# Kernel tuning notes

Hardware: AMD Instinct MI355X
Metric: run time of the kernel (lower is better)

Reference implementation:

```python
import jax, jax.numpy as jnp
import numpy as np

NEG = -1e30  # safe 'log zero' for fp32 (avoids -inf NaNs in grads)


def _ctc_loss(logits, targets, input_lengths, target_lengths):
    """PyTorch-semantics CTC loss: blank=0, reduction='mean', zero_infinity=True.
    logits: [B,T,C] (pre-log-softmax), targets: [B,S] padded, lengths: [B].
    """
    B, T, C = logits.shape
    S = targets.shape[1]
    L = 2 * S + 1  # extended target length (blanks interleaved)
    logp = jax.nn.log_softmax(logits, axis=-1)  # [B,T,C]

    # extended targets: blank, y1, blank, y2, ..., blank
    ext = jnp.zeros((B, L), jnp.int32).at[:, 1::2].set(targets.astype(jnp.int32))
    lp_ext = jnp.take_along_axis(
        logp, jnp.broadcast_to(ext[:, None, :], (B, T, L)), axis=2)  # [B,T,L]

    pos = jnp.arange(L)
    ext_m2 = jnp.pad(ext, ((0, 0), (2, 0)))[:, :L]
    can_skip = (ext != 0) & (ext != ext_m2) & (pos >= 2)  # [B,L]

    def shift(a, k):
        return jnp.pad(a, ((0, 0), (k, 0)), constant_values=NEG)[:, :L]

    def lse3(a, b, c):
        m = jnp.maximum(jnp.maximum(a, b), c)
        return m + jnp.log(jnp.exp(a - m) + jnp.exp(b - m) + jnp.exp(c - m))

    alpha0 = (jnp.full((B, L), NEG, logits.dtype)
              .at[:, 0].set(lp_ext[:, 0, 0])
              .at[:, 1].set(lp_ext[:, 0, 1]))

    def step(alpha, xs):
        lp_t, t = xs  # lp_t: [B,L]
        a2 = shift(alpha, 1)
        a3 = jnp.where(can_skip, shift(alpha, 2), NEG)
        new = lp_t + lse3(alpha, a2, a3)
        # freeze alpha once past each sample's input_length
        alpha = jnp.where((t < input_lengths)[:, None], new, alpha)
        return alpha, None

    lp_T = jnp.swapaxes(lp_ext, 0, 1)  # [T,B,L]
    alpha, _ = jax.lax.scan(step, alpha0, (lp_T[1:], jnp.arange(1, T)))

    i1 = (2 * target_lengths - 1).astype(jnp.int32)
    i2 = (2 * target_lengths).astype(jnp.int32)
    a_last = jnp.take_along_axis(alpha, i1[:, None], axis=1)[:, 0]
    a_blank = jnp.take_along_axis(alpha, i2[:, None], axis=1)[:, 0]
    loss = -jnp.logaddexp(a_last, a_blank)  # [B]
    loss = jnp.where(loss > 1e29, 0.0, loss)  # zero_infinity=True
    return jnp.mean(loss / target_lengths.astype(loss.dtype))


def setup_inputs() -> dict:
    key = jax.random.key(0)
    ks = jax.random.split(key, 8)
    B, T = 32, 2000
    C_err, S_err = 4, 50
    C_ph, S_ph = 64, 200
    error_logits = jax.random.normal(ks[0], (B, T, C_err), jnp.float32)
    phoneme_logits = jax.random.normal(ks[1], (B, T, C_ph), jnp.float32)
    # labels in [1, C): blank=0 never appears in targets
    error_targets = jax.random.randint(ks[2], (B, S_err), 1, C_err, jnp.int32)
    phoneme_targets = jax.random.randint(ks[3], (B, S_ph), 1, C_ph, jnp.int32)
    error_input_lengths = jax.random.randint(ks[4], (B,), T - T // 4, T + 1, jnp.int32)
    phoneme_input_lengths = jax.random.randint(ks[5], (B,), T - T // 4, T + 1, jnp.int32)
    error_target_lengths = jax.random.randint(ks[6], (B,), S_err // 2, S_err + 1, jnp.int32)
    phoneme_target_lengths = jax.random.randint(ks[7], (B,), S_ph // 2, S_ph + 1, jnp.int32)
    return {
        "error_logits": error_logits,
        "phoneme_logits": phoneme_logits,
        "error_targets": error_targets,
        "phoneme_targets": phoneme_targets,
        "error_input_lengths": error_input_lengths,
        "phoneme_input_lengths": phoneme_input_lengths,
        "error_target_lengths": error_target_lengths,
        "phoneme_target_lengths": phoneme_target_lengths,
    }


def reference(error_logits, phoneme_logits, error_targets, phoneme_targets,
              error_input_lengths, phoneme_input_lengths,
              error_target_lengths, phoneme_target_lengths):
    error_weight = 1.0
    phoneme_weight = 1.0
    error_loss = _ctc_loss(error_logits, error_targets,
                           error_input_lengths, error_target_lengths)
    phoneme_loss = _ctc_loss(phoneme_logits, phoneme_targets,
                             phoneme_input_lengths, phoneme_target_lengths)
    total_loss = error_weight * error_loss + phoneme_weight * phoneme_loss
    return total_loss
```

## Files before the change

### kernel.cpp

```cpp
#include <hip/hip_runtime.h>
#include <math.h>


static constexpr float  LOG2E = 1.4426950408889634f;
static constexpr double LN2D  = 0.6931471805599453;
static constexpr int GROWS = 2032;

#define DPP_WAVE_SHR1   0x138
#define DPP_ROW_SHR(n)  (0x110 | (n))
#define DPP_ROW_BCAST15 0x142
#define DPP_ROW_BCAST31 0x143

__device__ __forceinline__ float fexp2(float x) {
  return __builtin_amdgcn_exp2f(x);
}
__device__ __forceinline__ float flog2(float x) {
  return __builtin_amdgcn_logf(x);
}

__device__ __forceinline__ double dpp_shr1_f64(double x) {
  int lo = __double2loint(x), hi = __double2hiint(x);
  lo = __builtin_amdgcn_update_dpp(0, lo, DPP_WAVE_SHR1, 0xf, 0xf, true);
  hi = __builtin_amdgcn_update_dpp(0, hi, DPP_WAVE_SHR1, 0xf, 0xf, true);
  return __hiloint2double(hi, lo);
}

__device__ __forceinline__ int imax2(int a, int b) { return a > b ? a : b; }

__device__ __forceinline__ int wave_imax(int v) {
  v = imax2(v, __builtin_amdgcn_update_dpp(0, v, DPP_ROW_SHR(1), 0xf, 0xf, true));
  v = imax2(v, __builtin_amdgcn_update_dpp(0, v, DPP_ROW_SHR(2), 0xf, 0xf, true));
  v = imax2(v, __builtin_amdgcn_update_dpp(0, v, DPP_ROW_SHR(4), 0xf, 0xf, true));
  v = imax2(v, __builtin_amdgcn_update_dpp(0, v, DPP_ROW_SHR(8), 0xf, 0xf, true));
  v = imax2(v, __builtin_amdgcn_update_dpp(0, v, DPP_ROW_BCAST15, 0xf, 0xf, true));
  v = imax2(v, __builtin_amdgcn_update_dpp(0, v, DPP_ROW_BCAST31, 0xf, 0xf, true));
  return __builtin_amdgcn_readlane(v, 63);
}

__device__ __forceinline__ void wait_lgkm0() {
  __builtin_amdgcn_sched_barrier(0);
  __builtin_amdgcn_s_waitcnt(49279);
  __builtin_amdgcn_sched_barrier(0);
}

__device__ __forceinline__ void spin_fence() {
  __builtin_amdgcn_sched_barrier(0);
}


__global__ __launch_bounds__(256) void gather_ph_kernel(
    const float* __restrict__ ph_logits, const float* __restrict__ err_logits,
    const int* __restrict__ ph_tgt,
    float* __restrict__ Gph, float* __restrict__ Lpb_ph,
    float* __restrict__ Lpb_er, float* __restrict__ out) {
  const int bx = blockIdx.x, b = blockIdx.y;
  const int tid = threadIdx.x;
  const int lane = tid & 63, wv = tid >> 6;

  if (bx == 0 && b == 0 && tid == 0) *out = 0.f;

  if (wv == 0 && lane < 32) {
    const int t = bx * 32 + lane;
    if (t < 2000) {
      const float4 v = *(const float4*)(err_logits + ((size_t)b * 2000 + t) * 4);
      const float z0 = v.x * LOG2E;
      const float s = fexp2(z0) + fexp2(v.y * LOG2E) + fexp2(v.z * LOG2E) +
                      fexp2(v.w * LOG2E);
      Lpb_er[(size_t)b * GROWS + t] = z0 - flog2(s);
    }
  }

  const int* tb = ph_tgt + b * 200;
  int idx[4];
  float msk[4];
#pragma unroll
  for (int k = 0; k < 4; ++k) {
    const int si = lane * 4 + k;
    const int cls = (si < 200) ? tb[si] : 0;
    idx[k] = cls << 2;
    msk[k] = (si < 200) ? 1.0f : 0.0f;
  }
  const int t0 = (bx * 4 + wv) * 8;
  float z[8], e[8], s[8];
#pragma unroll
  for (int u = 0; u < 8; ++u) {
    const int t = t0 + u;
    const int tc = (t < 2000) ? t : 1999;
    z[u] = ph_logits[((size_t)b * 2000 + tc) * 64 + lane] * LOG2E;
    e[u] = fexp2(z[u]);
    s[u] = e[u];
  }
#pragma unroll
  for (int off = 32; off >= 1; off >>= 1) {
#pragma unroll
    for (int u = 0; u < 8; ++u) s[u] += __shfl_xor(s[u], off, 64);
  }
#pragma unroll
  for (int u = 0; u < 8; ++u) {
    const int t = t0 + u;
    if (t < 2000) {
      const float e0 = __int_as_float(
          __builtin_amdgcn_readlane(__float_as_int(e[u]), 0));
      const float inv0 = 1.0f / e0;
      float o[4];
#pragma unroll
      for (int k = 0; k < 4; ++k) {
        const float v = __int_as_float(
            __builtin_amdgcn_ds_bpermute(idx[k], __float_as_int(e[u])));
        o[k] = msk[k] * v * inv0;
      }
      *(float4*)(Gph + ((size_t)b * GROWS + t) * 256 + lane * 4) =
          make_float4(o[0], o[1], o[2], o[3]);
      if (lane == 0)
        Lpb_ph[(size_t)b * GROWS + t] = z[u] - flog2(s[u]);
    }
  }
}

template <int P> struct RowP { float v[P]; };

template <int P>
__device__ __forceinline__ void bl_renorm(double (&B)[P], double (&L)[P],
                                          int& K) {
  double mm = B[0];
#pragma unroll
  for (int k = 0; k < P; ++k) mm = fmax(fmax(mm, B[k]), L[k]);
  const int ex = (__double2hiint(mm) >> 20) & 0x7ff;
  const int emax = wave_imax(ex);
  if (emax > 0) {
    int d = 1523 - emax;
    if (d > 1023) d = 1023;
    if (d < -1022) d = -1022;
    const double sc = __hiloint2double((d + 1023) << 20, 0);
#pragma unroll
    for (int k = 0; k < P; ++k) { B[k] *= sc; L[k] *= sc; }
    K += d;
  }
}

template <int P>
__device__ __forceinline__ void bl_step(double (&B)[P], double (&L)[P],
                                        const double (&skipm)[P],
                                        const RowP<P>& f) {
  const double Lm1 = dpp_shr1_f64(L[P - 1]);
  double nB[P], nL[P];
#pragma unroll
  for (int k = 0; k < P; ++k) {
    const double Lp = (k >= 1) ? L[k - 1] : Lm1;
    nB[k] = B[k] + Lp;
    nL[k] = (double)f.v[k] * fma(skipm[k], Lp, B[k] + L[k]);
  }
#pragma unroll
  for (int k = 0; k < P; ++k) { B[k] = nB[k]; L[k] = nL[k]; }
}

template <int P>
__device__ __forceinline__ void bl_readout(double (&B)[P], double (&L)[P],
                                           int K, float spb, int tl,
                                           float* __restrict__ out,
                                           double* sa) {
  const int lane = threadIdx.x;
  double* saB = sa;
  double* saL = sa + 64 * P;
#pragma unroll
  for (int k = 0; k < P; ++k) {
    saB[lane * P + k] = B[k];
    saL[lane * P + k] = L[k];
  }
  wait_lgkm0();
  if (lane == 0) {
    const double a = saL[tl - 1] + saB[tl];
    float loss = (float)((double)K * LN2D - log(a) - (double)spb * LN2D);
    if (!(loss < 1e29f)) loss = 0.f;
    atomicAdd(out, loss / ((float)tl * 32.0f));
  }
}

__device__ __forceinline__ float spb_sum(const float* __restrict__ Lpb,
                                         int len) {
  const int lane = threadIdx.x;
  float spb = 0.f;
  for (int t0 = lane; t0 < len; t0 += 512) {
#pragma unroll
    for (int u = 0; u < 8; ++u) {
      const int t = t0 + u * 64;
      const int tc = (t < len) ? t : 0;
      const float v = Lpb[tc];
      spb += (t < len) ? v : 0.0f;
    }
  }
#pragma unroll
  for (int off = 32; off >= 1; off >>= 1) spb += __shfl_xor(spb, off, 64);
  return spb;
}

__device__ __forceinline__ void chain_ph(
    const float* __restrict__ Glab,
    const float* __restrict__ Lpb,
    const int* __restrict__ tb, int len, int tl,
    float* __restrict__ out, double* sa) {
  constexpr int P = 4, S = 200, LSTRIDE = 256;
  const int lane = threadIdx.x;

  const float spb = spb_sum(Lpb, len);

  double skipm[P];
#pragma unroll
  for (int k = 0; k < P; ++k) {
    const int s = lane * P + k;
    skipm[k] = (s >= 1 && s < S && tb[s] != tb[s - 1]) ? 1.0 : 0.0;
  }

  double B[P], L[P];
#pragma unroll
  for (int k = 0; k < P; ++k) { B[k] = 0.0; L[k] = 0.0; }
  {
    const float r0 = Glab[0];
    if (lane == 0) { B[0] = 1.0; L[0] = (double)r0; }
  }
  int K = 0;

  const float* gp = Glab + lane * P;
  const int ngroups = (len - 1) / 16;

  auto ldrow = [&](int t) {
    RowP<P> r;
    const float4 a = *(const float4*)(gp + (size_t)t * LSTRIDE);
    r.v[0] = a.x; r.v[1] = a.y; r.v[2] = a.z; r.v[3] = a.w;
    return r;
  };

  RowP<P> bufA[16], bufB[16];
  if (ngroups >= 1) {
#pragma unroll
    for (int u = 0; u < 16; ++u) bufA[u] = ldrow(1 + u);
  }
  if (ngroups >= 2) {
#pragma unroll
    for (int u = 0; u < 16; ++u) bufB[u] = ldrow(17 + u);
  }
  spin_fence();

  int g = 0;
  for (; g + 2 <= ngroups; g += 2) {
    bl_renorm<P>(B, L, K);
#pragma unroll
    for (int u = 0; u < 16; ++u) bl_step<P>(B, L, skipm, bufA[u]);
    {
      const int gn = (g + 2 < ngroups) ? (g + 2) : 0;
      const int tbase = 1 + gn * 16;
#pragma unroll
      for (int u = 0; u < 16; ++u) bufA[u] = ldrow(tbase + u);
    }
    spin_fence();
    bl_renorm<P>(B, L, K);
#pragma unroll
    for (int u = 0; u < 16; ++u) bl_step<P>(B, L, skipm, bufB[u]);
    {
      const int gn = (g + 3 < ngroups) ? (g + 3) : 0;
      const int tbase = 1 + gn * 16;
#pragma unroll
      for (int u = 0; u < 16; ++u) bufB[u] = ldrow(tbase + u);
    }
    spin_fence();
  }
  if (g < ngroups) {
    bl_renorm<P>(B, L, K);
#pragma unroll
    for (int u = 0; u < 16; ++u) bl_step<P>(B, L, skipm, bufA[u]);
    ++g;
  }

  {
    const int tstart = 1 + ngroups * 16;
    RowP<P> bufT[15];
#pragma unroll
    for (int u = 0; u < 15; ++u) {
      int t = tstart + u;
      if (t > len - 1) t = len - 1;
      bufT[u] = ldrow(t);
    }
#pragma unroll
    for (int u = 0; u < 15; ++u) {
      const int t = tstart + u;
      if (t < len) {
        if (u == 0) bl_renorm<P>(B, L, K);
        bl_step<P>(B, L, skipm, bufT[u]);
      }
    }
  }

  bl_readout<P>(B, L, K, spb, tl, out, sa);
}

__device__ __forceinline__ void chain_er(
    const float* __restrict__ zb,
    const float* __restrict__ Lpb,
    const int* __restrict__ tb, int len, int tl,
    float* __restrict__ out, double* sa) {
  constexpr int P = 1, S = 50;
  const int lane = threadIdx.x;

  const float spb = spb_sum(Lpb, len);

  const int c1 = tb[(lane < S) ? lane : (S - 1)];
  const float fmask = (lane < S) ? 1.0f : 0.0f;
  double skipm[P];
  skipm[0] = (lane >= 1 && lane < S && tb[lane] != tb[lane - 1]) ? 1.0 : 0.0;

  double B[P], L[P];
  B[0] = 0.0; L[0] = 0.0;
  const float4* zr = (const float4*)zb;
  {
    const float4 q0 = zr[0];
    const int c0 = tb[0];
    const float zc = (c0 == 1) ? q0.y : (c0 == 2) ? q0.z : q0.w;
    if (lane == 0) {
      B[0] = 1.0;
      L[0] = (double)fexp2((zc - q0.x) * LOG2E);
    }
  }
  int K = 0;
  const int ngroups = (len - 1) / 16;

  auto mkf = [&](float4 q) {
    RowP<P> f;
    const float zc = (c1 == 1) ? q.y : (c1 == 2) ? q.z : q.w;
    f.v[0] = fmask * fexp2((zc - q.x) * LOG2E);
    return f;
  };

  float4 bufA[16], bufB[16];
  if (ngroups >= 1) {
#pragma unroll
    for (int u = 0; u < 16; ++u) bufA[u] = zr[1 + u];
  }
  if (ngroups >= 2) {
#pragma unroll
    for (int u = 0; u < 16; ++u) bufB[u] = zr[17 + u];
  }
  spin_fence();

  int g = 0;
  for (; g + 2 <= ngroups; g += 2) {
    bl_renorm<P>(B, L, K);
#pragma unroll
    for (int u = 0; u < 16; ++u) {
      const RowP<P> f = mkf(bufA[u]);
      bl_step<P>(B, L, skipm, f);
    }
    {
      const int gn = (g + 2 < ngroups) ? (g + 2) : 0;
      const float4* nx = zr + 1 + (size_t)gn * 16;
#pragma unroll
      for (int u = 0; u < 16; ++u) bufA[u] = nx[u];
    }
    spin_fence();
    bl_renorm<P>(B, L, K);
#pragma unroll
    for (int u = 0; u < 16; ++u) {
      const RowP<P> f = mkf(bufB[u]);
      bl_step<P>(B, L, skipm, f);
    }
    {
      const int gn = (g + 3 < ngroups) ? (g + 3) : 0;
      const float4* nx = zr + 1 + (size_t)gn * 16;
#pragma unroll
      for (int u = 0; u < 16; ++u) bufB[u] = nx[u];
    }
    spin_fence();
  }
  if (g < ngroups) {
    bl_renorm<P>(B, L, K);
#pragma unroll
    for (int u = 0; u < 16; ++u) {
      const RowP<P> f = mkf(bufA[u]);
      bl_step<P>(B, L, skipm, f);
    }
    ++g;
  }

  {
    const int tstart = 1 + ngroups * 16;
    float4 bufT[15];
#pragma unroll
    for (int u = 0; u < 15; ++u) {
      int t = tstart + u;
      if (t > len - 1) t = len - 1;
      bufT[u] = zr[t];
    }
#pragma unroll
    for (int u = 0; u < 15; ++u) {
      const int t = tstart + u;
      if (t < len) {
        if (u == 0) bl_renorm<P>(B, L, K);
        const RowP<P> f = mkf(bufT[u]);
        bl_step<P>(B, L, skipm, f);
      }
    }
  }

  bl_readout<P>(B, L, K, spb, tl, out, sa);
}

__global__ __launch_bounds__(64, 1) void ctc_chains_pin_kernel(
    const float* __restrict__ Gph, const float* __restrict__ err_logits,
    const int* __restrict__ ph_tgt, const int* __restrict__ err_tgt,
    const int* __restrict__ err_il, const int* __restrict__ ph_il,
    const int* __restrict__ err_tl, const int* __restrict__ ph_tl,
    const float* __restrict__ Lpb_ph, const float* __restrict__ Lpb_er,
    float* __restrict__ out) {
  __shared__ double sa[512];
  const int blk = blockIdx.x;
  if (blk < 32) {
    int len = err_il[blk]; if (len > 2000) len = 2000;
    chain_er(err_logits + (size_t)blk * 2000 * 4,
             Lpb_er + (size_t)blk * GROWS, err_tgt + blk * 50, len,
             err_tl[blk], out, sa);
  } else {
    const int b = blk - 32;
    int len = ph_il[b]; if (len > 2000) len = 2000;
    chain_ph(Gph + (size_t)b * GROWS * 256,
             Lpb_ph + (size_t)b * GROWS, ph_tgt + b * 200, len,
             ph_tl[b], out, sa);
  }
}


__global__ __launch_bounds__(256) void softmax4_kernel(
    const float* __restrict__ x, float* __restrict__ p, int nrows) {
  int r = blockIdx.x * blockDim.x + threadIdx.x;
  if (r >= nrows) return;
  float4 v = *reinterpret_cast<const float4*>(x + (size_t)r * 4);
  float z0 = v.x * LOG2E, z1 = v.y * LOG2E, z2 = v.z * LOG2E, z3 = v.w * LOG2E;
  float m = fmaxf(fmaxf(z0, z1), fmaxf(z2, z3));
  float e0 = fexp2(z0 - m), e1 = fexp2(z1 - m);
  float e2 = fexp2(z2 - m), e3 = fexp2(z3 - m);
  float inv = 1.0f / (e0 + e1 + e2 + e3);
  float4 o;
  o.x = e0 * inv; o.y = e1 * inv; o.z = e2 * inv; o.w = e3 * inv;
  *reinterpret_cast<float4*>(p + (size_t)r * 4) = o;
}

__global__ __launch_bounds__(256) void softmax64_kernel(
    const float* __restrict__ x, float* __restrict__ p, int nrows) {
  int row = blockIdx.x * 4 + (threadIdx.x >> 6);
  int lane = threadIdx.x & 63;
  if (row >= nrows) return;
  float z = x[(size_t)row * 64 + lane] * LOG2E;
  float m = z;
#pragma unroll
  for (int off = 32; off >= 1; off >>= 1) m = fmaxf(m, __shfl_xor(m, off, 64));
  float e = fexp2(z - m);
  float s = e;
#pragma unroll
  for (int off = 32; off >= 1; off >>= 1) s += __shfl_xor(s, off, 64);
  p[(size_t)row * 64 + lane] = e * (1.0f / s);
}

template <int C, int S, int R>
__device__ __forceinline__ void ctc_chain_lin_fb(
    const float* __restrict__ p_b, const int* __restrict__ tgt_b,
    int len, int tl, float* __restrict__ out, double* sa) {
  constexpr int L = 2 * S + 1;
  const int lane = threadIdx.x;
  int idx[R];
  double skipm[R];
#pragma unroll
  for (int j = 0; j < R; ++j) {
    const int l = lane * R + j;
    int cls = 0;
    bool sk = false;
    if (l & 1) {
      const int s = (l - 1) >> 1;
      const int sc = (s < S) ? s : (S - 1);
      cls = tgt_b[sc];
      if (s >= 1 && s < S) sk = (cls != tgt_b[s - 1]);
    }
    idx[j] = cls * 4;
    skipm[j] = sk ? 1.0 : 0.0;
  }
  double alpha[R];
#pragma unroll
  for (int j = 0; j < R; ++j) {
    const int l = lane * R + j;
    alpha[j] = (l <= 1) ? (double)p_b[idx[j] >> 2] : 0.0;
  }
  int K = 0;
  const int cl = lane & (C - 1);
  float rv = p_b[(size_t)((1 < len - 1) ? 1 : (len - 1)) * C + cl];
  float pf[R];
#pragma unroll
  for (int j = 0; j < R; ++j)
    pf[j] = __int_as_float(__builtin_amdgcn_ds_bpermute(idx[j], __float_as_int(rv)));
  rv = p_b[(size_t)((2 < len - 1) ? 2 : (len - 1)) * C + cl];
  for (int t = 1; t < len; ++t) {
    if ((t & 31) == 0) {
      double m = alpha[0];
#pragma unroll
      for (int j = 1; j < R; ++j) m = fmax(m, alpha[j]);
#pragma unroll
      for (int off = 1; off < 64; off <<= 1) m = fmax(m, __shfl_xor(m, off, 64));
      const long long bits = __double_as_longlong(m);
      const int e = (int)((bits >> 52) & 0x7FF);
      if (e > 0) {
        const double sc = __longlong_as_double((long long)(2046 - e) << 52);
#pragma unroll
        for (int j = 0; j < R; ++j) alpha[j] *= sc;
        K += 1023 - e;
      }
    }
    const int tn = (t + 2 < len) ? (t + 2) : (len - 1);
    const float rvn = p_b[(size_t)tn * C + cl];
    float pfn[R];
#pragma unroll
    for (int j = 0; j < R; ++j)
      pfn[j] = __int_as_float(__builtin_amdgcn_ds_bpermute(idx[j], __float_as_int(rv)));
    double am1 = __shfl_up(alpha[R - 1], 1, 64);
    double am2 = __shfl_up(alpha[R - 2], 1, 64);
    if (lane == 0) { am1 = 0.0; am2 = 0.0; }
    double na[R];
#pragma unroll
    for (int j = 0; j < R; ++j) {
      const double a0 = alpha[j];
      const double a1 = (j >= 1) ? alpha[j - 1] : am1;
      const double a2 = (j >= 2) ? alpha[j - 2] : ((j == 1) ? am1 : am2);
      double s = a0 + a1;
      s = fma(skipm[j], a2, s);
      na[j] = (double)pf[j] * s;
    }
#pragma unroll
    for (int j = 0; j < R; ++j) alpha[j] = na[j];
#pragma unroll
    for (int j = 0; j < R; ++j) pf[j] = pfn[j];
    rv = rvn;
  }
#pragma unroll
  for (int j = 0; j < R; ++j) {
    const int l = lane * R + j;
    if (l < L) sa[l] = alpha[j];
  }
  __syncthreads();
  if (lane == 0) {
    const double a = sa[2 * tl - 1] + sa[2 * tl];
    float loss = (float)((double)K * LN2D - log(a));
    if (!(loss < 1e29f)) loss = 0.0f;
    atomicAdd(out, loss / ((float)tl * 32.0f));
  }
}

__global__ __launch_bounds__(64) void ctc_chains_fb_kernel(
    const float* __restrict__ p_err, const float* __restrict__ p_ph,
    const int* __restrict__ err_tgt, const int* __restrict__ ph_tgt,
    const int* __restrict__ err_il, const int* __restrict__ ph_il,
    const int* __restrict__ err_tl, const int* __restrict__ ph_tl,
    float* __restrict__ out) {
  __shared__ double sa[512];
  const int T = 2000;
  const int blk = blockIdx.x;
  if (blk < 32) {
    const int b = blk;
    int len = err_il[b]; if (len > T) len = T;
    ctc_chain_lin_fb<4, 50, 2>(p_err + (size_t)b * T * 4, err_tgt + b * 50, len,
                               err_tl[b], out, sa);
  } else {
    const int b = blk - 32;
    int len = ph_il[b]; if (len > T) len = T;
    ctc_chain_lin_fb<64, 200, 7>(p_ph + (size_t)b * T * 64, ph_tgt + b * 200,
                                 len, ph_tl[b], out, sa);
  }
}


extern "C" void kernel_launch(void* const* d_in, const int* in_sizes, int n_in,
                              void* d_out, int out_size, void* d_ws,
                              size_t ws_size, hipStream_t stream) {
  const float* err_logits = (const float*)d_in[0];
  const float* ph_logits  = (const float*)d_in[1];
  const int* err_tgt = (const int*)d_in[2];
  const int* ph_tgt  = (const int*)d_in[3];
  const int* err_il  = (const int*)d_in[4];
  const int* ph_il   = (const int*)d_in[5];
  const int* err_tl  = (const int*)d_in[6];
  const int* ph_tl   = (const int*)d_in[7];
  float* out = (float*)d_out;

  const size_t gph = (size_t)32 * GROWS * 256;
  const size_t lpb = (size_t)32 * GROWS;
  const size_t need = (gph + 2 * lpb) * sizeof(float);

  if (ws_size >= need) {
    float* Gph = (float*)d_ws;
    float* Lpb_ph = Gph + gph;
    float* Lpb_er = Lpb_ph + lpb;
    gather_ph_kernel<<<dim3(63, 32), 256, 0, stream>>>(
        ph_logits, err_logits, ph_tgt, Gph, Lpb_ph, Lpb_er, out);
    ctc_chains_pin_kernel<<<64, 64, 0, stream>>>(
        Gph, err_logits, ph_tgt, err_tgt, err_il, ph_il, err_tl, ph_tl,
        Lpb_ph, Lpb_er, out);
  } else {
    (void)hipMemsetAsync(d_out, 0, sizeof(float), stream);
    const int B = 32, T = 2000;
    const int rows = B * T;
    float* p_err = (float*)d_ws;
    float* p_ph  = p_err + (size_t)rows * 4;
    softmax4_kernel<<<(rows + 255) / 256, 256, 0, stream>>>(err_logits, p_err, rows);
    softmax64_kernel<<<(rows + 3) / 4, 256, 0, stream>>>(ph_logits, p_ph, rows);
    ctc_chains_fb_kernel<<<64, 64, 0, stream>>>(p_err, p_ph, err_tgt, ph_tgt,
                                                err_il, ph_il, err_tl, ph_tl, out);
  }
}
```

Before: 222.9 us.

## Split CTC recursion into concurrent forward and backward halves meeting at midpoint

Each block now runs two waves: one computes the alpha recursion over the first half of the time steps while the other runs a beta-style backward recursion over the second half. The two halves are combined with a dot product of the state vectors, with the renormalisation exponents added together. This roughly halves the serial dependency chain length per sequence, which dominates the chain kernel. It adds a backward step implementation, shared-memory exchange and a block barrier, and it risks numerical mismatch in the scaling bookkeeping.

```diff
diff --git a/kernel.cpp b/kernel.cpp
--- a/kernel.cpp
+++ b/kernel.cpp
@@ -6,6 +6,7 @@
 static constexpr double LN2D  = 0.6931471805599453;
 static constexpr int GROWS = 2032;
 
+#define DPP_WAVE_SHL1   0x130
 #define DPP_WAVE_SHR1   0x138
 #define DPP_ROW_SHR(n)  (0x110 | (n))
 #define DPP_ROW_BCAST15 0x142
@@ -22,6 +23,13 @@
   int lo = __double2loint(x), hi = __double2hiint(x);
   lo = __builtin_amdgcn_update_dpp(0, lo, DPP_WAVE_SHR1, 0xf, 0xf, true);
   hi = __builtin_amdgcn_update_dpp(0, hi, DPP_WAVE_SHR1, 0xf, 0xf, true);
+  return __hiloint2double(hi, lo);
+}
+
+__device__ __forceinline__ double dpp_shl1_f64(double x) {
+  int lo = __double2loint(x), hi = __double2hiint(x);
+  lo = __builtin_amdgcn_update_dpp(0, lo, DPP_WAVE_SHL1, 0xf, 0xf, true);
+  hi = __builtin_amdgcn_update_dpp(0, hi, DPP_WAVE_SHL1, 0xf, 0xf, true);
   return __hiloint2double(hi, lo);
 }
 
@@ -37,16 +45,6 @@
   return __builtin_amdgcn_readlane(v, 63);
 }
 
-__device__ __forceinline__ void wait_lgkm0() {
-  __builtin_amdgcn_sched_barrier(0);
-  __builtin_amdgcn_s_waitcnt(49279);
-  __builtin_amdgcn_sched_barrier(0);
-}
-
-__device__ __forceinline__ void spin_fence() {
-  __builtin_amdgcn_sched_barrier(0);
-}
-
 
 __global__ __launch_bounds__(256) void gather_ph_kernel(
     const float* __restrict__ ph_logits, const float* __restrict__ err_logits,
@@ -121,14 +119,14 @@
 
 template <int P>
 __device__ __forceinline__ void bl_renorm(double (&B)[P], double (&L)[P],
-                                          int& K) {
+                                          int& K, int tgt) {
   double mm = B[0];
 #pragma unroll
   for (int k = 0; k < P; ++k) mm = fmax(fmax(mm, B[k]), L[k]);
   const int ex = (__double2hiint(mm) >> 20) & 0x7ff;
   const int emax = wave_imax(ex);
   if (emax > 0) {
-    int d = 1523 - emax;
+    int d = tgt - emax;
     if (d > 1023) d = 1023;
     if (d < -1022) d = -1022;
     const double sc = __hiloint2double((d + 1023) << 20, 0);
@@ -155,30 +153,28 @@
 }
 
 template <int P>
-__device__ __forceinline__ void bl_readout(double (&B)[P], double (&L)[P],
-                                           int K, float spb, int tl,
-                                           float* __restrict__ out,
-                                           double* sa) {
-  const int lane = threadIdx.x;
-  double* saB = sa;
-  double* saL = sa + 64 * P;
+__device__ __forceinline__ void bl_step_bwd(double (&B)[P], double (&L)[P],
+                                            const double (&sknext)[P],
+                                            const RowP<P>& f) {
+  double w[P];
+#pragma unroll
+  for (int k = 0; k < P; ++k) w[k] = (double)f.v[k] * L[k];
+  const double wN = dpp_shl1_f64(w[0]);
+  const double BN = dpp_shl1_f64(B[0]);
+  double nB[P], nL[P];
 #pragma unroll
   for (int k = 0; k < P; ++k) {
-    saB[lane * P + k] = B[k];
-    saL[lane * P + k] = L[k];
-  }
-  wait_lgkm0();
-  if (lane == 0) {
-    const double a = saL[tl - 1] + saB[tl];
-    float loss = (float)((double)K * LN2D - log(a) - (double)spb * LN2D);
-    if (!(loss < 1e29f)) loss = 0.f;
-    atomicAdd(out, loss / ((float)tl * 32.0f));
-  }
+    const double wp1 = (k < P - 1) ? w[k + 1] : wN;
+    const double Bp1 = (k < P - 1) ? B[k + 1] : BN;
+    nB[k] = B[k] + w[k];
+    nL[k] = fma(sknext[k], wp1, w[k] + Bp1);
+  }
+#pragma unroll
+  for (int k = 0; k < P; ++k) { B[k] = nB[k]; L[k] = nL[k]; }
 }
 
 __device__ __forceinline__ float spb_sum(const float* __restrict__ Lpb,
-                                         int len) {
-  const int lane = threadIdx.x;
+                                         int len, int lane) {
   float spb = 0.f;
   for (int t0 = lane; t0 < len; t0 += 512) {
 #pragma unroll
@@ -194,34 +190,138 @@
   return spb;
 }
 
-__device__ __forceinline__ void chain_ph(
-    const float* __restrict__ Glab,
-    const float* __restrict__ Lpb,
-    const int* __restrict__ tb, int len, int tl,
-    float* __restrict__ out, double* sa) {
+template <int P, typename LdF, typename UseF>
+__device__ __forceinline__ void run_fwd(int nsteps, LdF ldrow, UseF use,
+                                        double (&B)[P], double (&L)[P],
+                                        const double (&sk)[P], int& K) {
+  using Buf = decltype(ldrow(1));
+  const int ng = nsteps / 16;
+  Buf bufA[16], bufB[16];
+  if (ng >= 1) {
+#pragma unroll
+    for (int u = 0; u < 16; ++u) bufA[u] = ldrow(1 + u);
+  }
+  if (ng >= 2) {
+#pragma unroll
+    for (int u = 0; u < 16; ++u) bufB[u] = ldrow(17 + u);
+  }
+  int g = 0;
+  for (; g + 2 <= ng; g += 2) {
+    bl_renorm<P>(B, L, K, 1523);
+    {
+      const int gn = (g + 2 < ng) ? (g + 2) : 0;
+#pragma unroll
+      for (int u = 0; u < 16; ++u) {
+        bl_step<P>(B, L, sk, use(bufA[u]));
+        bufA[u] = ldrow(1 + gn * 16 + u);
+      }
+    }
+    bl_renorm<P>(B, L, K, 1523);
+    {
+      const int gn = (g + 3 < ng) ? (g + 3) : 0;
+#pragma unroll
+      for (int u = 0; u < 16; ++u) {
+        bl_step<P>(B, L, sk, use(bufB[u]));
+        bufB[u] = ldrow(1 + gn * 16 + u);
+      }
+    }
+  }
+  if (g < ng) {
+    bl_renorm<P>(B, L, K, 1523);
+#pragma unroll
+    for (int u = 0; u < 16; ++u) bl_step<P>(B, L, sk, use(bufA[u]));
+    ++g;
+  }
+  {
+    const int tstart = 1 + ng * 16;
+    Buf bufT[15];
+#pragma unroll
+    for (int u = 0; u < 15; ++u) {
+      int t = tstart + u;
+      if (t > nsteps) t = (nsteps > 0) ? nsteps : 1;
+      bufT[u] = ldrow(t);
+    }
+#pragma unroll
+    for (int u = 0; u < 15; ++u) {
+      if (tstart + u <= nsteps) {
+        if (u == 0) bl_renorm<P>(B, L, K, 1523);
+        bl_step<P>(B, L, sk, use(bufT[u]));
+      }
+    }
+  }
+}
+
+template <int P, typename LdF, typename UseF>
+__device__ __forceinline__ void run_bwd(int len, int M, LdF ldrow, UseF use,
+                                        double (&B)[P], double (&L)[P],
+                                        const double (&sk)[P], int& K) {
+  using Buf = decltype(ldrow(1));
+  const int ng = M / 16;
+  Buf bufA[16], bufB[16];
+  if (ng >= 1) {
+#pragma unroll
+    for (int u = 0; u < 16; ++u) bufA[u] = ldrow(len - 1 - u);
+  }
+  if (ng >= 2) {
+#pragma unroll
+    for (int u = 0; u < 16; ++u) bufB[u] = ldrow(len - 17 - u);
+  }
+  int g = 0;
+  for (; g + 2 <= ng; g += 2) {
+    bl_renorm<P>(B, L, K, 1023);
+    {
+      const int jb = (g + 2 < ng) ? (g + 2) * 16 : 0;
+#pragma unroll
+      for (int u = 0; u < 16; ++u) {
+        bl_step_bwd<P>(B, L, sk, use(bufA[u]));
+        bufA[u] = ldrow(len - 1 - jb - u);
+      }
+    }
+    bl_renorm<P>(B, L, K, 1023);
+    {
+      const int jb = (g + 3 < ng) ? (g + 3) * 16 : 0;
+#pragma unroll
+      for (int u = 0; u < 16; ++u) {
+        bl_step_bwd<P>(B, L, sk, use(bufB[u]));
+        bufB[u] = ldrow(len - 1 - jb - u);
+      }
+    }
+  }
+  if (g < ng) {
+    bl_renorm<P>(B, L, K, 1023);
+#pragma unroll
+    for (int u = 0; u < 16; ++u) bl_step_bwd<P>(B, L, sk, use(bufA[u]));
+    ++g;
+  }
+  {
+    const int jstart = ng * 16;
+    Buf bufT[15];
+#pragma unroll
+    for (int u = 0; u < 15; ++u) {
+      int j = jstart + u;
+      if (j > M - 1) j = (M > 0) ? (M - 1) : 0;
+      bufT[u] = ldrow(len - 1 - j);
+    }
+#pragma unroll
+    for (int u = 0; u < 15; ++u) {
+      if (jstart + u < M) {
+        if (u == 0) bl_renorm<P>(B, L, K, 1023);
+        bl_step_bwd<P>(B, L, sk, use(bufT[u]));
+      }
+    }
+  }
+}
+
+__device__ __forceinline__ void chain_ph_fb(
+    const float* __restrict__ Glab, const float* __restrict__ Lpb,
+    const int* __restrict__ tb, int len, int tl, float* __restrict__ out,
+    double* sBb, double* sLb, int* sKb) {
   constexpr int P = 4, S = 200, LSTRIDE = 256;
-  const int lane = threadIdx.x;
-
-  const float spb = spb_sum(Lpb, len);
-
-  double skipm[P];
-#pragma unroll
-  for (int k = 0; k < P; ++k) {
-    const int s = lane * P + k;
-    skipm[k] = (s >= 1 && s < S && tb[s] != tb[s - 1]) ? 1.0 : 0.0;
-  }
-
-  double B[P], L[P];
-#pragma unroll
-  for (int k = 0; k < P; ++k) { B[k] = 0.0; L[k] = 0.0; }
-  {
-    const float r0 = Glab[0];
-    if (lane == 0) { B[0] = 1.0; L[0] = (double)r0; }
-  }
-  int K = 0;
-
+  const int tid = threadIdx.x;
+  const int wave = tid >> 6, lane = tid & 63;
+  const int t_mid = len >> 1;
+  const int M = (len - 1) - t_mid;
   const float* gp = Glab + lane * P;
-  const int ngroups = (len - 1) / 16;
 
   auto ldrow = [&](int t) {
     RowP<P> r;
@@ -229,200 +329,156 @@
     r.v[0] = a.x; r.v[1] = a.y; r.v[2] = a.z; r.v[3] = a.w;
     return r;
   };
-
-  RowP<P> bufA[16], bufB[16];
-  if (ngroups >= 1) {
-#pragma unroll
-    for (int u = 0; u < 16; ++u) bufA[u] = ldrow(1 + u);
-  }
-  if (ngroups >= 2) {
-#pragma unroll
-    for (int u = 0; u < 16; ++u) bufB[u] = ldrow(17 + u);
-  }
-  spin_fence();
-
-  int g = 0;
-  for (; g + 2 <= ngroups; g += 2) {
-    bl_renorm<P>(B, L, K);
-#pragma unroll
-    for (int u = 0; u < 16; ++u) bl_step<P>(B, L, skipm, bufA[u]);
+  auto use_id = [](const RowP<P>& r) { return r; };
+
+  float spb = 0.f;
+  double B[P], L[P];
+  int Kf = 0;
+
+  if (wave == 0) {
+    spb = spb_sum(Lpb, len, lane);
+    double skipm[P];
+#pragma unroll
+    for (int k = 0; k < P; ++k) {
+      const int s = lane * P + k;
+      skipm[k] = (s >= 1 && s < S && tb[s] != tb[s - 1]) ? 1.0 : 0.0;
+    }
+#pragma unroll
+    for (int k = 0; k < P; ++k) { B[k] = 0.0; L[k] = 0.0; }
     {
-      const int gn = (g + 2 < ngroups) ? (g + 2) : 0;
-      const int tbase = 1 + gn * 16;
-#pragma unroll
-      for (int u = 0; u < 16; ++u) bufA[u] = ldrow(tbase + u);
-    }
-    spin_fence();
-    bl_renorm<P>(B, L, K);
-#pragma unroll
-    for (int u = 0; u < 16; ++u) bl_step<P>(B, L, skipm, bufB[u]);
-    {
-      const int gn = (g + 3 < ngroups) ? (g + 3) : 0;
-      const int tbase = 1 + gn * 16;
-#pragma unroll
-      for (int u = 0; u < 16; ++u) bufB[u] = ldrow(tbase + u);
-    }
-    spin_fence();
-  }
-  if (g < ngroups) {
-    bl_renorm<P>(B, L, K);
-#pragma unroll
-    for (int u = 0; u < 16; ++u) bl_step<P>(B, L, skipm, bufA[u]);
-    ++g;
-  }
-
-  {
-    const int tstart = 1 + ngroups * 16;
-    RowP<P> bufT[15];
-#pragma unroll
-    for (int u = 0; u < 15; ++u) {
-      int t = tstart + u;
-      if (t > len - 1) t = len - 1;
-      bufT[u] = ldrow(t);
-    }
-#pragma unroll
-    for (int u = 0; u < 15; ++u) {
-      const int t = tstart + u;
-      if (t < len) {
-        if (u == 0) bl_renorm<P>(B, L, K);
-        bl_step<P>(B, L, skipm, bufT[u]);
-      }
-    }
-  }
-
-  bl_readout<P>(B, L, K, spb, tl, out, sa);
-}
-
-__device__ __forceinline__ void chain_er(
-    const float* __restrict__ zb,
-    const float* __restrict__ Lpb,
-    const int* __restrict__ tb, int len, int tl,
-    float* __restrict__ out, double* sa) {
+      const float r0 = Glab[0];
+      if (lane == 0) { B[0] = 1.0; L[0] = (double)r0; }
+    }
+    run_fwd<P>(t_mid, ldrow, use_id, B, L, skipm, Kf);
+  } else {
+    double sknext[P];
+#pragma unroll
+    for (int k = 0; k < P; ++k) {
+      const int s = lane * P + k;
+      sknext[k] = (s + 1 < S && tb[s + 1] != tb[s]) ? 1.0 : 0.0;
+    }
+    double Bb[P], Lb[P];
+#pragma unroll
+    for (int k = 0; k < P; ++k) {
+      const int s = lane * P + k;
+      Bb[k] = (s == tl) ? 1.0 : 0.0;
+      Lb[k] = (s == tl - 1) ? 1.0 : 0.0;
+    }
+    int Kb = 0;
+    run_bwd<P>(len, M, ldrow, use_id, Bb, Lb, sknext, Kb);
+#pragma unroll
+    for (int k = 0; k < P; ++k) {
+      sBb[lane * P + k] = Bb[k];
+      sLb[lane * P + k] = Lb[k];
+    }
+    if (lane == 0) *sKb = Kb;
+  }
+  __syncthreads();
+  if (wave == 0) {
+    double dot = 0.0;
+#pragma unroll
+    for (int k = 0; k < P; ++k)
+      dot += B[k] * sBb[lane * P + k] + L[k] * sLb[lane * P + k];
+#pragma unroll
+    for (int off = 32; off >= 1; off >>= 1) dot += __shfl_xor(dot, off, 64);
+    if (lane == 0) {
+      const int K2 = Kf + *sKb;
+      float loss = (float)((double)K2 * LN2D - log(dot) - (double)spb * LN2D);
+      if (!(loss < 1e29f)) loss = 0.f;
+      atomicAdd(out, loss / ((float)tl * 32.0f));
+    }
+  }
+}
+
+__device__ __forceinline__ void chain_er_fb(
+    const float* __restrict__ zb, const float* __restrict__ Lpb,
+    const int* __restrict__ tb, int len, int tl, float* __restrict__ out,
+    double* sBb, double* sLb, int* sKb) {
   constexpr int P = 1, S = 50;
-  const int lane = threadIdx.x;
-
-  const float spb = spb_sum(Lpb, len);
+  const int tid = threadIdx.x;
+  const int wave = tid >> 6, lane = tid & 63;
+  const int t_mid = len >> 1;
+  const int M = (len - 1) - t_mid;
+  const float4* zr = (const float4*)zb;
 
   const int c1 = tb[(lane < S) ? lane : (S - 1)];
   const float fmask = (lane < S) ? 1.0f : 0.0f;
-  double skipm[P];
-  skipm[0] = (lane >= 1 && lane < S && tb[lane] != tb[lane - 1]) ? 1.0 : 0.0;
-
-  double B[P], L[P];
-  B[0] = 0.0; L[0] = 0.0;
-  const float4* zr = (const float4*)zb;
-  {
-    const float4 q0 = zr[0];
-    const int c0 = tb[0];
-    const float zc = (c0 == 1) ? q0.y : (c0 == 2) ? q0.z : q0.w;
-    if (lane == 0) {
-      B[0] = 1.0;
-      L[0] = (double)fexp2((zc - q0.x) * LOG2E);
-    }
-  }
-  int K = 0;
-  const int ngroups = (len - 1) / 16;
-
-  auto mkf = [&](float4 q) {
+
+  auto ldrow = [&](int t) { return zr[t]; };
+  auto mkf = [&](const float4& q) {
     RowP<P> f;
     const float zc = (c1 == 1) ? q.y : (c1 == 2) ? q.z : q.w;
     f.v[0] = fmask * fexp2((zc - q.x) * LOG2E);
     return f;
   };
 
-  float4 bufA[16], bufB[16];
-  if (ngroups >= 1) {
-#pragma unroll
-    for (int u = 0; u < 16; ++u) bufA[u] = zr[1 + u];
-  }
-  if (ngroups >= 2) {
-#pragma unroll
-    for (int u = 0; u < 16; ++u) bufB[u] = zr[17 + u];
-  }
-  spin_fence();
-
-  int g = 0;
-  for (; g + 2 <= ngroups; g += 2) {
-    bl_renorm<P>(B, L, K);
-#pragma unroll
-    for (int u = 0; u < 16; ++u) {
-      const RowP<P> f = mkf(bufA[u]);
-      bl_step<P>(B, L, skipm, f);
-    }
+  float spb = 0.f;
+  double B[P], L[P];
+  int Kf = 0;
+
+  if (wave == 0) {
+    spb = spb_sum(Lpb, len, lane);
+    double skipm[P];
+    skipm[0] =
+        (lane >= 1 && lane < S && tb[lane] != tb[lane - 1]) ? 1.0 : 0.0;
+    B[0] = 0.0; L[0] = 0.0;
     {
-      const int gn = (g + 2 < ngroups) ? (g + 2) : 0;
-      const float4* nx = zr + 1 + (size_t)gn * 16;
-#pragma unroll
-      for (int u = 0; u < 16; ++u) bufA[u] = nx[u];
-    }
-    spin_fence();
-    bl_renorm<P>(B, L, K);
-#pragma unroll
-    for (int u = 0; u < 16; ++u) {
-      const RowP<P> f = mkf(bufB[u]);
-      bl_step<P>(B, L, skipm, f);
-    }
-    {
-      const int gn = (g + 3 < ngroups) ? (g + 3) : 0;
-      const float4* nx = zr + 1 + (size_t)gn * 16;
-#pragma unroll
-      for (int u = 0; u < 16; ++u) bufB[u] = nx[u];
-    }
-    spin_fence();
-  }
-  if (g < ngroups) {
-    bl_renorm<P>(B, L, K);
-#pragma unroll
-    for (int u = 0; u < 16; ++u) {
-      const RowP<P> f = mkf(bufA[u]);
-      bl_step<P>(B, L, skipm, f);
-    }
-    ++g;
-  }
-
-  {
-    const int tstart = 1 + ngroups * 16;
-    float4 bufT[15];
-#pragma unroll
-    for (int u = 0; u < 15; ++u) {
-      int t = tstart + u;
-      if (t > len - 1) t = len - 1;
-      bufT[u] = zr[t];
-    }
-#pragma unroll
-    for (int u = 0; u < 15; ++u) {
-      const int t = tstart + u;
-      if (t < len) {
-        if (u == 0) bl_renorm<P>(B, L, K);
-        const RowP<P> f = mkf(bufT[u]);
-        bl_step<P>(B, L, skipm, f);
-      }
-    }
-  }
-
-  bl_readout<P>(B, L, K, spb, tl, out, sa);
-}
-
-__global__ __launch_bounds__(64, 1) void ctc_chains_pin_kernel(
+      const float4 q0 = zr[0];
+      const int c0 = tb[0];
+      const float zc = (c0 == 1) ? q0.y : (c0 == 2) ? q0.z : q0.w;
+      if (lane == 0) {
+        B[0] = 1.0;
+        L[0] = (double)fexp2((zc - q0.x) * LOG2E);
+      }
+    }
+    run_fwd<P>(t_mid, ldrow, mkf, B, L, skipm, Kf);
+  } else {
+    double sknext[P];
+    sknext[0] = (lane + 1 < S && tb[lane + 1] != tb[lane]) ? 1.0 : 0.0;
+    double Bb[P], Lb[P];
+    Bb[0] = (lane == tl) ? 1.0 : 0.0;
+    Lb[0] = (lane == tl - 1) ? 1.0 : 0.0;
+    int Kb = 0;
+    run_bwd<P>(len, M, ldrow, mkf, Bb, Lb, sknext, Kb);
+    sBb[lane] = Bb[0];
+    sLb[lane] = Lb[0];
+    if (lane == 0) *sKb = Kb;
+  }
+  __syncthreads();
+  if (wave == 0) {
+    double dot = B[0] * sBb[lane] + L[0] * sLb[lane];
+#pragma unroll
+    for (int off = 32; off >= 1; off >>= 1) dot += __shfl_xor(dot, off, 64);
+    if (lane == 0) {
+      const int K2 = Kf + *sKb;
+      float loss = (float)((double)K2 * LN2D - log(dot) - (double)spb * LN2D);
+      if (!(loss < 1e29f)) loss = 0.f;
+      atomicAdd(out, loss / ((float)tl * 32.0f));
+    }
+  }
+}
+
+__global__ __launch_bounds__(128) void ctc_chains_fbsplit_kernel(
     const float* __restrict__ Gph, const float* __restrict__ err_logits,
     const int* __restrict__ ph_tgt, const int* __restrict__ err_tgt,
     const int* __restrict__ err_il, const int* __restrict__ ph_il,
     const int* __restrict__ err_tl, const int* __restrict__ ph_tl,
     const float* __restrict__ Lpb_ph, const float* __restrict__ Lpb_er,
     float* __restrict__ out) {
-  __shared__ double sa[512];
+  __shared__ double sBb[256], sLb[256];
+  __shared__ int sKb;
   const int blk = blockIdx.x;
   if (blk < 32) {
     int len = err_il[blk]; if (len > 2000) len = 2000;
-    chain_er(err_logits + (size_t)blk * 2000 * 4,
-             Lpb_er + (size_t)blk * GROWS, err_tgt + blk * 50, len,
-             err_tl[blk], out, sa);
+    chain_er_fb(err_logits + (size_t)blk * 2000 * 4,
+                Lpb_er + (size_t)blk * GROWS, err_tgt + blk * 50, len,
+                err_tl[blk], out, sBb, sLb, &sKb);
   } else {
     const int b = blk - 32;
     int len = ph_il[b]; if (len > 2000) len = 2000;
-    chain_ph(Gph + (size_t)b * GROWS * 256,
-             Lpb_ph + (size_t)b * GROWS, ph_tgt + b * 200, len,
-             ph_tl[b], out, sa);
+    chain_ph_fb(Gph + (size_t)b * GROWS * 256,
+                Lpb_ph + (size_t)b * GROWS, ph_tgt + b * 200, len,
+                ph_tl[b], out, sBb, sLb, &sKb);
   }
 }
 
@@ -595,7 +651,7 @@
     float* Lpb_er = Lpb_ph + lpb;
     gather_ph_kernel<<<dim3(63, 32), 256, 0, stream>>>(
         ph_logits, err_logits, ph_tgt, Gph, Lpb_ph, Lpb_er, out);
-    ctc_chains_pin_kernel<<<64, 64, 0, stream>>>(
+    ctc_chains_fbsplit_kernel<<<64, 128, 0, stream>>>(
         Gph, err_logits, ph_tgt, err_tgt, err_il, ph_il, err_tl, ph_tl,
         Lpb_ph, Lpb_er, out);
   } else {
```

Result: faster. 204.2 us (-8.4%).
